# Kernel tuning notes

Hardware: AMD Instinct MI355X
Metric: run time of the kernel (lower is better)

Reference implementation:

```python
import jax, jax.numpy as jnp
import numpy as np

VOCAB = 100000
PAD_ID = 0
INTEREST_ID = 1
B, S, D = 16, 200, 128

def setup_inputs() -> dict:
    key = jax.random.key(0)
    ks = jax.random.split(key, 10)
    sc = 0.05
    return {
        "x": jax.random.normal(ks[0], (B, S, D), jnp.float32),
        "x_ids": jax.random.randint(ks[1], (B, S), 0, VOCAB),
        "Wq": jax.random.normal(ks[2], (D, D), jnp.float32) * sc,
        "bq": jax.random.normal(ks[3], (D,), jnp.float32) * sc,
        "Wk": jax.random.normal(ks[4], (D, D), jnp.float32) * sc,
        "bk": jax.random.normal(ks[5], (D,), jnp.float32) * sc,
        "Wv": jax.random.normal(ks[6], (D, 1), jnp.float32) * sc,
        "bv": jax.random.normal(ks[7], (1,), jnp.float32) * sc,
        "Wec": jax.random.normal(ks[8], (2 * D, VOCAB), jnp.float32) * sc,
        "bec": jax.random.normal(ks[9], (VOCAB,), jnp.float32) * sc,
    }

def reference(x, x_ids, Wq, bq, Wk, bk, Wv, bv, Wec, bec):
    # mask: valid (non-pad, non-interest) positions  (B,S)
    mask = (x_ids != PAD_ID) & (x_ids != INTEREST_ID)
    # additive attention pooling (explore_proj=True)
    q = jnp.einsum('bsd,de->bse', x, Wq) + bq            # (B,S,D)
    k = jnp.einsum('bd,de->be', x[:, 0, :], Wk) + bk      # (B,D), broadcast over S
    features = jnp.tanh(q + k[:, None, :])                # (B,S,D)
    scores = jnp.einsum('bsd,do->bso', features, Wv)[..., 0] + bv[0]  # (B,S)
    scores = jax.nn.softmax(scores, axis=-1)
    c_s = jnp.einsum('bsd,bs->bd', x, scores)             # (B,D)
    h_t = x[:, 0, :]                                      # (B,D)
    c_s = jnp.concatenate([h_t, c_s], axis=-1)            # (B,2D)
    p_explore = c_s @ Wec + bec                           # (B,V)
    # explore_mask: histogram of masked ids over vocab.
    # Equivalent to bmm(mask, one_hot(x_ids)) but O(B*S) scatter instead of O(B*S*V).
    explore_mask = jnp.zeros((x.shape[0], VOCAB), jnp.float32)
    batch_idx = jnp.arange(x.shape[0])[:, None]           # (B,1)
    explore_mask = explore_mask.at[batch_idx, x_ids].add(mask.astype(jnp.float32))
    p_explore = jnp.where(explore_mask > 0, -jnp.inf, p_explore)
    return jax.nn.softmax(p_explore, axis=-1)
```

## Files before the change

kernel.cpp:

```cpp
#include <hip/hip_runtime.h>
#include <cstdint>
#include <cstddef>
#include <math.h>

#define B 16
#define S 200
#define D 128
#define VOCAB 100000
#define V4 (VOCAB / 4)
#define SCH 8
#define VTILE 256
#define NBLK ((VOCAB + VTILE - 1) / VTILE)
#define CH 16
#define NCH (2 * D / CH)

__global__ __launch_bounds__(128) void k_scores(
    const float* __restrict__ x,
    const float* __restrict__ Wq, const float* __restrict__ bq,
    const float* __restrict__ Wk, const float* __restrict__ bk,
    const float* __restrict__ Wv, const float* __restrict__ bv,
    float* __restrict__ scores)
{
  const int b  = blockIdx.x / (S / SCH);
  const int s0 = (blockIdx.x % (S / SCH)) * SCH;
  const int e  = threadIdx.x;

  __shared__ float lx[SCH][D];
  __shared__ float l0[D];
  __shared__ float sred[2][SCH];

  l0[e] = x[(size_t)b * S * D + e];
  #pragma unroll
  for (int i = 0; i < SCH; i++) lx[i][e] = x[((size_t)b * S + s0 + i) * D + e];
  __syncthreads();

  float q[SCH];
  const float bqe = bq[e];
  #pragma unroll
  for (int i = 0; i < SCH; i++) q[i] = bqe;
  float kk = bk[e];

  for (int d = 0; d < D; d++) {
    const float wq = Wq[d * D + e];
    const float wk = Wk[d * D + e];
    const float x0 = l0[d];
    kk += x0 * wk;
    #pragma unroll
    for (int i = 0; i < SCH; i++) q[i] += lx[i][d] * wq;
  }

  const float wv  = Wv[e];
  const float bv0 = bv[0];
  #pragma unroll
  for (int i = 0; i < SCH; i++) {
    float val = tanhf(q[i] + kk) * wv;
    #pragma unroll
    for (int off = 32; off > 0; off >>= 1) val += __shfl_down(val, off, 64);
    if ((e & 63) == 0) sred[e >> 6][i] = val;
  }
  __syncthreads();
  if (e < SCH) scores[b * S + s0 + e] = sred[0][e] + sred[1][e] + bv0;
}

__global__ __launch_bounds__(512) void k_csum(
    const float* __restrict__ x, const float* __restrict__ scores,
    float* __restrict__ cvec)
{
  const int b = blockIdx.x;
  const int t = threadIdx.x;
  __shared__ float pr[S];
  __shared__ float redm[9];
  __shared__ float reds[9];
  __shared__ float cpart[3][D];

  float v = (t < S) ? scores[b * S + t] : -INFINITY;
  float m = v;
  #pragma unroll
  for (int off = 32; off > 0; off >>= 1) m = fmaxf(m, __shfl_down(m, off, 64));
  if ((t & 63) == 0) redm[t >> 6] = m;
  __syncthreads();
  if (t == 0) {
    float mm = redm[0];
    #pragma unroll
    for (int i = 1; i < 8; i++) mm = fmaxf(mm, redm[i]);
    redm[8] = mm;
  }
  __syncthreads();
  const float mx = redm[8];

  float e = (t < S) ? expf(v - mx) : 0.f;
  float s = e;
  #pragma unroll
  for (int off = 32; off > 0; off >>= 1) s += __shfl_down(s, off, 64);
  if ((t & 63) == 0) reds[t >> 6] = s;
  __syncthreads();
  if (t == 0) {
    float ss = 0.f;
    #pragma unroll
    for (int i = 0; i < 8; i++) ss += reds[i];
    reds[8] = ss;
  }
  __syncthreads();
  const float inv = 1.0f / reds[8];
  if (t < S) pr[t] = e * inv;
  __syncthreads();

  const int d = t & 127;
  const int sq = t >> 7;
  float acc = 0.f;
  const float* xb = x + ((size_t)b * S + sq * 50) * D + d;
  #pragma unroll 5
  for (int s2 = 0; s2 < 50; s2++) acc += pr[sq * 50 + s2] * xb[s2 * D];
  if (sq) cpart[sq - 1][d] = acc;
  __syncthreads();
  if (sq == 0) {
    cvec[d * B + b]       = x[(size_t)b * S * D + d];
    cvec[(D + d) * B + b] = acc + cpart[0][d] + cpart[1][d] + cpart[2][d];
  }
}

__global__ __launch_bounds__(256, 2) void k_gemv(
    const float* __restrict__ cvec, const float* __restrict__ Wec,
    const float* __restrict__ bec, float* __restrict__ out,
    float* __restrict__ partial)
{
  __shared__ __align__(16) char arena[49152];
  float (*wbuf)[CH][VTILE] = (float (*)[CH][VTILE])arena;
  float* cl = (float*)(arena + 32768);

  const int t    = threadIdx.x;
  const int lane = t & 63;
  const int dq   = __builtin_amdgcn_readfirstlane(t >> 6);

  {
    const float4* src = (const float4*)cvec;
    float4* dst = (float4*)cl;
    #pragma unroll
    for (int i = 0; i < 4; i++) dst[t + 256 * i] = src[t + 256 * i];
  }

  const int vbase = blockIdx.x * VTILE;
  const int v4    = blockIdx.x * 64 + lane;
  const bool valid = (v4 < V4);
  const int v4c   = valid ? v4 : (V4 - 1);
  const int laneoff = (vbase + lane * 4 + 3 < VOCAB) ? lane * 4 : 0;

#define STAGE(bufi, c)                                                      \
  { _Pragma("unroll")                                                       \
    for (int r = 0; r < 4; r++) {                                           \
      const int d = (c) * CH + dq * 4 + r;                                  \
      const float* gp = Wec + (size_t)d * VOCAB + vbase + laneoff;          \
      float* lp = &wbuf[bufi][dq * 4 + r][0];                               \
      __builtin_amdgcn_global_load_lds(                                     \
          (const __attribute__((address_space(1))) void*)gp,                \
          (__attribute__((address_space(3))) void*)lp, 16, 0, 0);           \
    } }

  float4 acc[16];
  #pragma unroll
  for (int i = 0; i < 16; i++) acc[i] = make_float4(0.f, 0.f, 0.f, 0.f);

  STAGE(0, 0)
  __syncthreads();

  int cur = 0;
  for (int c = 0; c < NCH; c++) {
    if (c < NCH - 1) STAGE(cur ^ 1, c + 1)
    #pragma unroll
    for (int r = 0; r < 4; r++) {
      const float4 w = ((const float4*)&wbuf[cur][dq * 4 + r][0])[lane];
      const float* cj = cl + (c * CH + dq * 4 + r) * 16;
      #pragma unroll
      for (int bb = 0; bb < 16; bb++) {
        const float cc = cj[bb];
        acc[bb].x = fmaf(w.x, cc, acc[bb].x);
        acc[bb].y = fmaf(w.y, cc, acc[bb].y);
        acc[bb].z = fmaf(w.z, cc, acc[bb].z);
        acc[bb].w = fmaf(w.w, cc, acc[bb].w);
      }
    }
    __syncthreads();
    cur ^= 1;
  }
#undef STAGE

  float2* redp = (float2*)arena;
#define RED(q, l, b) redp[(((q) * 64 + (l)) * 17) + (b)]

  const float4 be4 = ((const float4*)bec)[v4c];
  float psum[4] = {0.f, 0.f, 0.f, 0.f};

  #pragma unroll
  for (int bb = 0; bb < 16; bb++)
    RED(dq, lane, bb) = make_float2(acc[bb].x, acc[bb].y);
  __syncthreads();
  #pragma unroll
  for (int i = 0; i < 4; i++) {
    const int bb = dq * 4 + i;
    const float2 r0 = RED(0, lane, bb), r1 = RED(1, lane, bb);
    const float2 r2 = RED(2, lane, bb), r3 = RED(3, lane, bb);
    const float sx = r0.x + r1.x + r2.x + r3.x;
    const float sy = r0.y + r1.y + r2.y + r3.y;
    const float e0 = valid ? __expf(sx + be4.x) : 0.f;
    const float e1 = valid ? __expf(sy + be4.y) : 0.f;
    if (valid)
      *(float2*)&out[(size_t)bb * VOCAB + (size_t)v4 * 4] = make_float2(e0, e1);
    psum[i] += e0 + e1;
  }
  __syncthreads();

  #pragma unroll
  for (int bb = 0; bb < 16; bb++)
    RED(dq, lane, bb) = make_float2(acc[bb].z, acc[bb].w);
  __syncthreads();
  #pragma unroll
  for (int i = 0; i < 4; i++) {
    const int bb = dq * 4 + i;
    const float2 r0 = RED(0, lane, bb), r1 = RED(1, lane, bb);
    const float2 r2 = RED(2, lane, bb), r3 = RED(3, lane, bb);
    const float sz = r0.x + r1.x + r2.x + r3.x;
    const float sw = r0.y + r1.y + r2.y + r3.y;
    const float e2 = valid ? __expf(sz + be4.z) : 0.f;
    const float e3 = valid ? __expf(sw + be4.w) : 0.f;
    if (valid)
      *(float2*)&out[(size_t)bb * VOCAB + (size_t)v4 * 4 + 2] = make_float2(e2, e3);
    psum[i] += e2 + e3;
  }
#undef RED

  #pragma unroll
  for (int i = 0; i < 4; i++) {
    float s = psum[i];
    #pragma unroll
    for (int off = 32; off > 0; off >>= 1) s += __shfl_down(s, off, 64);
    if (lane == 0) partial[blockIdx.x * 16 + dq * 4 + i] = s;
  }
}

__global__ __launch_bounds__(256) void k_fix_inv(
    const int* __restrict__ ids, float* __restrict__ out,
    const float* __restrict__ partial, float* __restrict__ inv)
{
  const int t = threadIdx.x;
  __shared__ float corr[16];
  __shared__ float sred[256];

  if (t < 16) corr[t] = 0.f;
  __syncthreads();

  for (int i = t; i < B * S; i += 256) {
    const int id = ids[i];
    if (id > 1) {
      const int b = i / S;
      const float old = atomicExch(&out[(size_t)b * VOCAB + id], 0.f);
      atomicAdd(&corr[b], -old);
    }
  }

  float s = 0.f;
  #pragma unroll 4
  for (int j = (t >> 4); j < NBLK; j += 16) s += partial[j * 16 + (t & 15)];
  sred[t] = s;
  __syncthreads();

  if (t < 16) {
    float tot = 0.f;
    #pragma unroll
    for (int c = 0; c < 16; c++) tot += sred[c * 16 + t];
    inv[t] = 1.0f / (tot + corr[t]);
  }
}

__global__ __launch_bounds__(256) void k_norm(float* __restrict__ out,
                                              const float* __restrict__ inv)
{
  const int b  = blockIdx.y;
  const int i4 = blockIdx.x * 256 + threadIdx.x;
  const float iv = inv[b];
  if (i4 < V4) {
    float4* p = (float4*)out + (size_t)b * V4 + i4;
    float4 q = *p;
    q.x *= iv; q.y *= iv; q.z *= iv; q.w *= iv;
    *p = q;
  }
}

extern "C" void kernel_launch(void* const* d_in, const int* in_sizes, int n_in,
                              void* d_out, int out_size, void* d_ws, size_t ws_size,
                              hipStream_t stream)
{
  const float* x   = (const float*)d_in[0];
  const int*   ids = (const int*)d_in[1];
  const float* Wq  = (const float*)d_in[2];
  const float* bq  = (const float*)d_in[3];
  const float* Wk  = (const float*)d_in[4];
  const float* bk  = (const float*)d_in[5];
  const float* Wv  = (const float*)d_in[6];
  const float* bv  = (const float*)d_in[7];
  const float* Wec = (const float*)d_in[8];
  const float* bec = (const float*)d_in[9];
  float* out = (float*)d_out;
  float* ws  = (float*)d_ws;

  float* scores  = ws;
  float* cvec    = ws + 3200;
  float* partial = ws + 7296;
  float* inv     = ws + 13552;

  k_scores <<<dim3(B * (S / SCH)), dim3(128), 0, stream>>>(x, Wq, bq, Wk, bk, Wv, bv, scores);
  k_csum   <<<dim3(B),             dim3(512), 0, stream>>>(x, scores, cvec);
  k_gemv   <<<dim3(NBLK),          dim3(256), 0, stream>>>(cvec, Wec, bec, out, partial);
  k_fix_inv<<<dim3(1),             dim3(256), 0, stream>>>(ids, out, partial, inv);
  k_norm   <<<dim3((V4 + 255) / 256, B), dim3(256), 0, stream>>>(out, inv);
}
```

Before: 66.42 us.

## Fuse id masking into GEMV epilogue and fold sum reduction into normalize

```diff
diff --git a/kernel.cpp b/kernel.cpp
--- a/kernel.cpp
+++ b/kernel.cpp
@@ -121,12 +121,13 @@
 
 __global__ __launch_bounds__(256, 2) void k_gemv(
     const float* __restrict__ cvec, const float* __restrict__ Wec,
-    const float* __restrict__ bec, float* __restrict__ out,
-    float* __restrict__ partial)
+    const float* __restrict__ bec, const int* __restrict__ ids,
+    float* __restrict__ out, float* __restrict__ partial)
 {
   __shared__ __align__(16) char arena[49152];
   float (*wbuf)[CH][VTILE] = (float (*)[CH][VTILE])arena;
   float* cl = (float*)(arena + 32768);
+  __shared__ unsigned mbit[B * 8];
 
   const int t    = threadIdx.x;
   const int lane = t & 63;
@@ -138,6 +139,7 @@
     #pragma unroll
     for (int i = 0; i < 4; i++) dst[t + 256 * i] = src[t + 256 * i];
   }
+  if (t < B * 8) mbit[t] = 0u;
 
   const int vbase = blockIdx.x * VTILE;
   const int v4    = blockIdx.x * 64 + lane;
@@ -161,6 +163,15 @@
   for (int i = 0; i < 16; i++) acc[i] = make_float4(0.f, 0.f, 0.f, 0.f);
 
   STAGE(0, 0)
+
+  for (int i = t; i < B * S; i += 256) {
+    const int id = ids[i];
+    if (id > 1 && id >= vbase && id < vbase + VTILE) {
+      const int lv = id - vbase;
+      atomicOr(&mbit[(i / S) * 8 + (lv >> 5)], 1u << (lv & 31));
+    }
+  }
+
   __syncthreads();
 
   int cur = 0;
@@ -186,8 +197,10 @@
 
   float2* redp = (float2*)arena;
 #define RED(q, l, b) redp[(((q) * 64 + (l)) * 17) + (b)]
+#define MASKED(bb, lv) ((mbit[(bb) * 8 + ((lv) >> 5)] >> ((lv) & 31)) & 1u)
 
   const float4 be4 = ((const float4*)bec)[v4c];
+  const int lv0 = lane * 4;
   float psum[4] = {0.f, 0.f, 0.f, 0.f};
 
   #pragma unroll
@@ -201,10 +214,12 @@
     const float2 r2 = RED(2, lane, bb), r3 = RED(3, lane, bb);
     const float sx = r0.x + r1.x + r2.x + r3.x;
     const float sy = r0.y + r1.y + r2.y + r3.y;
-    const float e0 = valid ? __expf(sx + be4.x) : 0.f;
-    const float e1 = valid ? __expf(sy + be4.y) : 0.f;
-    if (valid)
+    float e0 = 0.f, e1 = 0.f;
+    if (valid) {
+      e0 = MASKED(bb, lv0 + 0) ? 0.f : __expf(sx + be4.x);
+      e1 = MASKED(bb, lv0 + 1) ? 0.f : __expf(sy + be4.y);
       *(float2*)&out[(size_t)bb * VOCAB + (size_t)v4 * 4] = make_float2(e0, e1);
+    }
     psum[i] += e0 + e1;
   }
   __syncthreads();
@@ -220,13 +235,16 @@
     const float2 r2 = RED(2, lane, bb), r3 = RED(3, lane, bb);
     const float sz = r0.x + r1.x + r2.x + r3.x;
     const float sw = r0.y + r1.y + r2.y + r3.y;
-    const float e2 = valid ? __expf(sz + be4.z) : 0.f;
-    const float e3 = valid ? __expf(sw + be4.w) : 0.f;
-    if (valid)
+    float e2 = 0.f, e3 = 0.f;
+    if (valid) {
+      e2 = MASKED(bb, lv0 + 2) ? 0.f : __expf(sz + be4.z);
+      e3 = MASKED(bb, lv0 + 3) ? 0.f : __expf(sw + be4.w);
       *(float2*)&out[(size_t)bb * VOCAB + (size_t)v4 * 4 + 2] = make_float2(e2, e3);
+    }
     psum[i] += e2 + e3;
   }
 #undef RED
+#undef MASKED
 
   #pragma unroll
   for (int i = 0; i < 4; i++) {
@@ -237,46 +255,22 @@
   }
 }
 
-__global__ __launch_bounds__(256) void k_fix_inv(
-    const int* __restrict__ ids, float* __restrict__ out,
-    const float* __restrict__ partial, float* __restrict__ inv)
-{
-  const int t = threadIdx.x;
-  __shared__ float corr[16];
-  __shared__ float sred[256];
-
-  if (t < 16) corr[t] = 0.f;
-  __syncthreads();
-
-  for (int i = t; i < B * S; i += 256) {
-    const int id = ids[i];
-    if (id > 1) {
-      const int b = i / S;
-      const float old = atomicExch(&out[(size_t)b * VOCAB + id], 0.f);
-      atomicAdd(&corr[b], -old);
-    }
-  }
+__global__ __launch_bounds__(256) void k_norm(float* __restrict__ out,
+                                              const float* __restrict__ partial)
+{
+  const int b  = blockIdx.y;
+  const int t  = threadIdx.x;
+  __shared__ float red[4];
 
   float s = 0.f;
-  #pragma unroll 4
-  for (int j = (t >> 4); j < NBLK; j += 16) s += partial[j * 16 + (t & 15)];
-  sred[t] = s;
-  __syncthreads();
-
-  if (t < 16) {
-    float tot = 0.f;
-    #pragma unroll
-    for (int c = 0; c < 16; c++) tot += sred[c * 16 + t];
-    inv[t] = 1.0f / (tot + corr[t]);
-  }
-}
-
-__global__ __launch_bounds__(256) void k_norm(float* __restrict__ out,
-                                              const float* __restrict__ inv)
-{
-  const int b  = blockIdx.y;
-  const int i4 = blockIdx.x * 256 + threadIdx.x;
-  const float iv = inv[b];
+  for (int j = t; j < NBLK; j += 256) s += partial[j * 16 + b];
+  #pragma unroll
+  for (int off = 32; off > 0; off >>= 1) s += __shfl_down(s, off, 64);
+  if ((t & 63) == 0) red[t >> 6] = s;
+  __syncthreads();
+  const float iv = 1.0f / (red[0] + red[1] + red[2] + red[3]);
+
+  const int i4 = blockIdx.x * 256 + t;
   if (i4 < V4) {
     float4* p = (float4*)out + (size_t)b * V4 + i4;
     float4 q = *p;
@@ -305,11 +299,9 @@
   float* scores  = ws;
   float* cvec    = ws + 3200;
   float* partial = ws + 7296;
-  float* inv     = ws + 13552;
 
   k_scores <<<dim3(B * (S / SCH)), dim3(128), 0, stream>>>(x, Wq, bq, Wk, bk, Wv, bv, scores);
   k_csum   <<<dim3(B),             dim3(512), 0, stream>>>(x, scores, cvec);
-  k_gemv   <<<dim3(NBLK),          dim3(256), 0, stream>>>(cvec, Wec, bec, out, partial);
-  k_fix_inv<<<dim3(1),             dim3(256), 0, stream>>>(ids, out, partial, inv);
-  k_norm   <<<dim3((V4 + 255) / 256, B), dim3(256), 0, stream>>>(out, inv);
-}
+  k_gemv   <<<dim3(NBLK),          dim3(256), 0, stream>>>(cvec, Wec, bec, ids, out, partial);
+  k_norm   <<<dim3((V4 + 255) / 256, B), dim3(256), 0, stream>>>(out, partial);
+}
```

Result: faster. 57.27 us (-13.8%).
